# Optimization experiments

Measured on AMD Instinct MI355X. Metric: run time of the kernel, lower is better.

The kernel has to match this reference:

```python
import jax, jax.numpy as jnp
import numpy as np

B, D, H, E, TOPK = 65536, 1024, 512, 8, 2
LN_EPS = 1e-5
LB_WEIGHT = 0.01


def setup_inputs() -> dict:
    key = jax.random.key(0)
    ks = jax.random.split(key, 5)
    x = jax.random.normal(ks[0], (B, D), dtype=jnp.float32)
    W1 = jax.random.normal(ks[1], (D, H), dtype=jnp.float32) * 0.02
    b1 = jnp.zeros((H,), dtype=jnp.float32)
    ln_w = jnp.ones((H,), dtype=jnp.float32)
    ln_b = jnp.zeros((H,), dtype=jnp.float32)
    W2 = jax.random.normal(ks[2], (H, E), dtype=jnp.float32) * 0.02
    b2 = jnp.zeros((E,), dtype=jnp.float32)
    return {"x": x, "W1": W1, "b1": b1, "ln_w": ln_w, "ln_b": ln_b, "W2": W2, "b2": b2}


def _gate_logits(x, W1, b1, ln_w, ln_b, W2, b2):
    h = x @ W1 + b1                     # [B, H]
    mu = jnp.mean(h, axis=-1, keepdims=True)
    var = jnp.mean(jnp.square(h - mu), axis=-1, keepdims=True)
    h = (h - mu) * jax.lax.rsqrt(var + LN_EPS) * ln_w + ln_b
    h = jax.nn.gelu(h, approximate=False)  # torch nn.GELU default = exact erf
    return h @ W2 + b2                  # [B, E]


def reference(x, W1, b1, ln_w, ln_b, W2, b2):
    logits = _gate_logits(x, W1, b1, ln_w, ln_b, W2, b2)
    # sparse top-K routing (eval mode: no exploration noise)
    vals, idx = jax.lax.top_k(logits, TOPK)           # [B, K]
    rows = jnp.arange(logits.shape[0])[:, None]
    sparse = jnp.full_like(logits, -jnp.inf).at[rows, idx].set(vals)
    weights = jax.nn.softmax(sparse, axis=-1)         # zeros off top-k
    # Switch-style load-balance loss
    f = (weights > 0).astype(weights.dtype).mean(axis=0)  # fraction routed per expert
    P = weights.mean(axis=0)                              # mean gate prob per expert
    lb_loss = LB_WEIGHT * (E * jnp.sum(f * P))
    return weights, lb_loss
```

## Files before the change

kernel.cpp:

```cpp
#include <hip/hip_runtime.h>
#include <cstdint>
#include <cstddef>


typedef _Float16 f16;
typedef _Float16 f16x8 __attribute__((ext_vector_type(8)));
typedef float f32x4 __attribute__((ext_vector_type(4)));

#define B_ROWS 65536
#define D_DIM 1024
#define H_DIM 512
#define E_DIM 8
#define BM 64
#define BK 32
#define THREADS 256
#define NCHUNK 32
#define LDPX 40
#define SLABH 2560
#define BUFH 5120
#define IMG_CH (H_DIM * BK)
#define IMG_TOTAL (32 * IMG_CH)
#define GACC_OFF ((size_t)2 * IMG_TOTAL * sizeof(f16))

__global__ void prep_split(const float* __restrict__ W1,
                           f16* __restrict__ wh, f16* __restrict__ wl) {
  int id = blockIdx.x * 256 + threadIdx.x;
  int h = id & (H_DIM - 1);
  int kg = id >> 9;
  int c = kg >> 2;
  int kk0 = (kg & 3) * 8;
  int k0 = kg * 8;
  f16x8 hv, lv;
#pragma unroll
  for (int j = 0; j < 8; ++j) {
    float v = W1[(size_t)(k0 + j) * H_DIM + h] * 64.0f;
    f16 hi = (f16)v;
    hv[j] = hi;
    lv[j] = (f16)((v - (float)hi) * 256.0f);
  }
  size_t o = (size_t)c * IMG_CH + (size_t)h * BK + kk0;
  *(f16x8*)&wh[o] = hv;
  *(f16x8*)&wl[o] = lv;
}

__global__ void zero_acc(float* __restrict__ acc) {
  if (threadIdx.x < 16) acc[threadIdx.x] = 0.0f;
}

__global__ __launch_bounds__(THREADS, 2) void fused_main(
    const float* __restrict__ x,
    const f16* __restrict__ wh, const f16* __restrict__ wl,
    const float* __restrict__ b1, const float* __restrict__ lnw,
    const float* __restrict__ lnb, const float* __restrict__ W2,
    const float* __restrict__ b2, float* __restrict__ out,
    float* __restrict__ gacc) {
  __shared__ __align__(16) char pool[35584];
  f16* sx = (f16*)pool;

  const int tid = threadIdx.x;
  const int lane = tid & 63;
  const int wv = tid >> 6;
  const int l15 = lane & 15;
  const int l4 = lane >> 4;
  const int64_t row0 = (int64_t)blockIdx.x * BM;

  const int srow = tid >> 2;
  const int koff = (tid & 3) * 8;
  const int swo = srow * LDPX + koff;
  const float* xbase = x + (row0 + srow) * D_DIM + koff;

  const f16* whp = wh + (wv * 128 + l15) * BK + l4 * 8;

  f32x4 acc[4][8];
#pragma unroll
  for (int m = 0; m < 4; ++m)
#pragma unroll
    for (int n = 0; n < 8; ++n) acc[m][n] = (f32x4){0.f, 0.f, 0.f, 0.f};

  f16x8 setB[2][8];

#define ISSUE(si, C, half)                                                    \
  do {                                                                        \
    const f16* p = whp + (size_t)((C) & 31) * IMG_CH + (half) * 2048;         \
    setB[si][0] = *(const f16x8*)(p);                                         \
    setB[si][1] = *(const f16x8*)(p + 512);                                   \
    setB[si][2] = *(const f16x8*)(p + 1024);                                  \
    setB[si][3] = *(const f16x8*)(p + 1536);                                  \
    setB[si][4] = *(const f16x8*)(p + IMG_TOTAL);                             \
    setB[si][5] = *(const f16x8*)(p + IMG_TOTAL + 512);                       \
    setB[si][6] = *(const f16x8*)(p + IMG_TOTAL + 1024);                      \
    setB[si][7] = *(const f16x8*)(p + IMG_TOTAL + 1536);                      \
  } while (0)

#define CH_M(si, NH, bufv, MM)                                                \
  do {                                                                        \
    const int ao = (bufv)*BUFH + ((MM)*16 + l15) * LDPX + l4 * 8;             \
    f16x8 ah = *(const f16x8*)&sx[ao];                                        \
    f16x8 al = *(const f16x8*)&sx[ao + SLABH];                                \
    f16x8 ahs;                                                                \
    _Pragma("unroll") for (int q = 0; q < 8; ++q) ahs[q] =                    \
        ah[q] * (f16)0.00390625f;                                             \
    _Pragma("unroll") for (int n = 0; n < 4; ++n)                             \
      acc[MM][(NH)*4 + n] = __builtin_amdgcn_mfma_f32_16x16x32_f16(           \
          ah, setB[si][n], acc[MM][(NH)*4 + n], 0, 0, 0);                     \
    _Pragma("unroll") for (int n = 0; n < 4; ++n)                             \
      acc[MM][(NH)*4 + n] = __builtin_amdgcn_mfma_f32_16x16x32_f16(           \
          al, setB[si][n], acc[MM][(NH)*4 + n], 0, 0, 0);                     \
    _Pragma("unroll") for (int n = 0; n < 4; ++n)                             \
      acc[MM][(NH)*4 + n] = __builtin_amdgcn_mfma_f32_16x16x32_f16(           \
          ahs, setB[si][4 + n], acc[MM][(NH)*4 + n], 0, 0, 0);                \
  } while (0)

#define HALF(si, NH, bufv)                                                    \
  do {                                                                        \
    __builtin_amdgcn_s_setprio(1);                                            \
    CH_M(si, NH, bufv, 0);                                                    \
    CH_M(si, NH, bufv, 1);                                                    \
    CH_M(si, NH, bufv, 2);                                                    \
    CH_M(si, NH, bufv, 3);                                                    \
    __builtin_amdgcn_s_setprio(0);                                            \
  } while (0)

#define WRITE_SLAB(bufv)                                                      \
  do {                                                                        \
    float vv[8] = {xv0.x, xv0.y, xv0.z, xv0.w, xv1.x, xv1.y, xv1.z, xv1.w};   \
    f16x8 hv, lv;                                                             \
    _Pragma("unroll") for (int q = 0; q < 8; ++q) {                           \
      float t = vv[q] * 64.0f;                                                \
      f16 hh = (f16)t;                                                        \
      hv[q] = hh;                                                             \
      lv[q] = (f16)(t - (float)hh);                                           \
    }                                                                         \
    *(f16x8*)&sx[(bufv)*BUFH + swo] = hv;                                     \
    *(f16x8*)&sx[(bufv)*BUFH + SLABH + swo] = lv;                             \
  } while (0)

#define SLAB_BARRIER()                                                        \
  do {                                                                        \
    asm volatile("s_waitcnt lgkmcnt(0)" ::: "memory");                        \
    __builtin_amdgcn_s_barrier();                                             \
    __builtin_amdgcn_sched_barrier(0);                                        \
  } while (0)

  float4 xv0 = *(const float4*)(xbase);
  float4 xv1 = *(const float4*)(xbase + 4);
  WRITE_SLAB(0);
  ISSUE(0, 0, 0);
  ISSUE(1, 0, 1);
  xv0 = *(const float4*)(xbase + 32);
  xv1 = *(const float4*)(xbase + 36);
  SLAB_BARRIER();

  for (int c = 0; c < NCHUNK; ++c) {
    const int buf = c & 1;
    HALF(0, 0, buf);
    ISSUE(0, c + 1, 0);
    HALF(1, 1, buf);
    ISSUE(1, c + 1, 1);
    WRITE_SLAB(buf ^ 1);
    xv0 = *(const float4*)(xbase + ((c + 2) & 31) * 32);
    xv1 = *(const float4*)(xbase + ((c + 2) & 31) * 32 + 4);
    SLAB_BARRIER();
  }
#undef ISSUE
#undef CH_M
#undef HALF
#undef WRITE_SLAB
#undef SLAB_BARRIER
  __syncthreads();

  float* eW2T = (float*)pool;
  float* eStat = (float*)(pool + 24576);
  float* eLog = (float*)(pool + 26624);
  float* eMu = (float*)(pool + 34816);
  float* eRs = (float*)(pool + 35072);
  float* eFP = (float*)(pool + 35328);

  for (int i = tid; i < H_DIM; i += THREADS) {
    float4 wa = *(const float4*)&W2[i * 8];
    float4 wb = *(const float4*)&W2[i * 8 + 4];
    *(float4*)&eW2T[i * 12] = wa;
    *(float4*)&eW2T[i * 12 + 4] = wb;
  }
  if (tid < 16) eFP[tid] = 0.0f;

  float bb[8], lw[8], lb[8];
#pragma unroll
  for (int n = 0; n < 8; ++n) {
    int col = wv * 128 + n * 16 + l15;
    bb[n] = b1[col] * 4096.0f;
    lw[n] = lnw[col];
    lb[n] = lnb[col];
#pragma unroll
    for (int m = 0; m < 4; ++m)
#pragma unroll
      for (int r = 0; r < 4; ++r) acc[m][n][r] += bb[n];
  }

#pragma unroll
  for (int m = 0; m < 4; ++m) {
    float s1[4] = {0, 0, 0, 0};
    float s2[4] = {0, 0, 0, 0};
#pragma unroll
    for (int n = 0; n < 8; ++n)
#pragma unroll
      for (int r = 0; r < 4; ++r) {
        float vv = acc[m][n][r];
        s1[r] += vv;
        s2[r] = fmaf(vv, vv, s2[r]);
      }
#pragma unroll
    for (int d = 1; d < 16; d <<= 1)
#pragma unroll
      for (int r = 0; r < 4; ++r) {
        s1[r] += __shfl_xor(s1[r], d);
        s2[r] += __shfl_xor(s2[r], d);
      }
    if (l15 == 0) {
      int rb = m * 16 + l4 * 4;
#pragma unroll
      for (int r = 0; r < 4; ++r) {
        eStat[(wv * 64 + rb + r) * 2 + 0] = s1[r];
        eStat[(wv * 64 + rb + r) * 2 + 1] = s2[r];
      }
    }
  }
  __syncthreads();
  if (tid < BM) {
    float s1 = 0.0f, s2 = 0.0f;
#pragma unroll
    for (int w = 0; w < 4; ++w) {
      s1 += eStat[(w * 64 + tid) * 2 + 0];
      s2 += eStat[(w * 64 + tid) * 2 + 1];
    }
    float mu = s1 * (1.0f / 512.0f);
    float var = s2 * (1.0f / 512.0f) - mu * mu;
    eMu[tid] = mu;
    eRs[tid] = 1.0f / sqrtf(var + (1e-5f * 4096.0f * 4096.0f));
  }
  __syncthreads();

#pragma unroll
  for (int m = 0; m < 4; ++m) {
    int rb = m * 16 + l4 * 4;
#pragma unroll
    for (int r = 0; r < 4; ++r) {
      float mu_r = eMu[rb + r];
      float rs_r = eRs[rb + r];
      float lg[8];
#pragma unroll
      for (int e = 0; e < 8; ++e) lg[e] = 0.0f;
#pragma unroll
      for (int n = 0; n < 8; ++n) {
        int col = wv * 128 + n * 16 + l15;
        float hn = (acc[m][n][r] - mu_r) * rs_r;
        float y = fmaf(hn, lw[n], lb[n]);
        float g = 0.5f * y * (1.0f + erff(y * 0.70710678118654752440f));
        float4 w0 = *(const float4*)&eW2T[col * 12];
        float4 w1 = *(const float4*)&eW2T[col * 12 + 4];
        lg[0] = fmaf(g, w0.x, lg[0]);
        lg[1] = fmaf(g, w0.y, lg[1]);
        lg[2] = fmaf(g, w0.z, lg[2]);
        lg[3] = fmaf(g, w0.w, lg[3]);
        lg[4] = fmaf(g, w1.x, lg[4]);
        lg[5] = fmaf(g, w1.y, lg[5]);
        lg[6] = fmaf(g, w1.z, lg[6]);
        lg[7] = fmaf(g, w1.w, lg[7]);
      }
#pragma unroll
      for (int d = 1; d < 16; d <<= 1)
#pragma unroll
        for (int e = 0; e < 8; ++e) lg[e] += __shfl_xor(lg[e], d);
      if (l15 == 0) {
#pragma unroll
        for (int e = 0; e < 8; ++e) eLog[(wv * 64 + rb + r) * 8 + e] = lg[e];
      }
    }
  }
  __syncthreads();

  if (tid < BM) {
    float v[8];
#pragma unroll
    for (int e = 0; e < 8; ++e) {
      float s = b2[e];
#pragma unroll
      for (int w = 0; w < 4; ++w) s += eLog[(w * 64 + tid) * 8 + e];
      v[e] = s;
    }
    float m1 = v[0];
    int i1 = 0;
#pragma unroll
    for (int e = 1; e < 8; ++e)
      if (v[e] > m1) { m1 = v[e]; i1 = e; }
    float m2 = -3.0e38f;
    int i2 = -1;
#pragma unroll
    for (int e = 0; e < 8; ++e)
      if (e != i1 && v[e] > m2) { m2 = v[e]; i2 = e; }
    float dd = expf(m2 - m1);
    float inv = 1.0f / (1.0f + dd);
    float wA = inv, wB = dd * inv;
    float o[8];
#pragma unroll
    for (int e = 0; e < 8; ++e)
      o[e] = (e == i1) ? wA : ((e == i2) ? wB : 0.0f);
    float4* op = (float4*)&out[(row0 + tid) * 8];
    op[0] = (float4){o[0], o[1], o[2], o[3]};
    op[1] = (float4){o[4], o[5], o[6], o[7]};
    atomicAdd(&eFP[i1], 1.0f);
    atomicAdd(&eFP[i2], 1.0f);
    atomicAdd(&eFP[8 + i1], wA);
    atomicAdd(&eFP[8 + i2], wB);
  }
  __syncthreads();
  if (tid < 16) atomicAdd(&gacc[tid], eFP[tid]);
}

__global__ void lb_final(const float* __restrict__ gacc, float* __restrict__ out) {
  if (threadIdx.x == 0) {
    const float invB = 1.0f / 65536.0f;
    float s = 0.0f;
#pragma unroll
    for (int e = 0; e < 8; ++e) s += (gacc[e] * invB) * (gacc[8 + e] * invB);
    out[(size_t)B_ROWS * E_DIM] = 0.01f * 8.0f * s;
  }
}

extern "C" void kernel_launch(void* const* d_in, const int* in_sizes, int n_in,
                              void* d_out, int out_size, void* d_ws, size_t ws_size,
                              hipStream_t stream) {
  (void)in_sizes; (void)n_in; (void)out_size; (void)ws_size;
  const float* x = (const float*)d_in[0];
  const float* W1 = (const float*)d_in[1];
  const float* b1 = (const float*)d_in[2];
  const float* lnw = (const float*)d_in[3];
  const float* lnb = (const float*)d_in[4];
  const float* W2 = (const float*)d_in[5];
  const float* b2 = (const float*)d_in[6];
  float* out = (float*)d_out;
  f16* wh = (f16*)d_ws;
  f16* wl = wh + IMG_TOTAL;
  float* gacc = (float*)((char*)d_ws + GACC_OFF);

  zero_acc<<<1, 64, 0, stream>>>(gacc);
  prep_split<<<(D_DIM * H_DIM / 8) / 256, 256, 0, stream>>>(W1, wh, wl);
  fused_main<<<B_ROWS / BM, THREADS, 0, stream>>>(x, wh, wl, b1, lnw, lnb, W2, b2,
                                                  out, gacc);
  lb_final<<<1, 64, 0, stream>>>(gacc, out);
}
```

Before: 242.4 us.

## Load x directly into per-wave registers, dropping LDS staging and barriers

Each wave now loads its own A-operand fragments of x straight from global memory and splits them into high/low fp16 in registers, instead of cooperatively staging x through double-buffered LDS with a barrier per chunk. This removes the LDS writes and reads and the per-chunk block synchronisation. The cost is that all four waves redundantly load the same 64 rows of x (4x global/L2 traffic), and the loads are no longer prefetched a chunk ahead, so their latency may be exposed before the MFMAs.

```diff
diff --git a/kernel.cpp b/kernel.cpp
--- a/kernel.cpp
+++ b/kernel.cpp
@@ -15,9 +15,6 @@
 #define BK 32
 #define THREADS 256
 #define NCHUNK 32
-#define LDPX 40
-#define SLABH 2560
-#define BUFH 5120
 #define IMG_CH (H_DIM * BK)
 #define IMG_TOTAL (32 * IMG_CH)
 #define GACC_OFF ((size_t)2 * IMG_TOTAL * sizeof(f16))
@@ -55,7 +52,6 @@
     const float* __restrict__ b2, float* __restrict__ out,
     float* __restrict__ gacc) {
   __shared__ __align__(16) char pool[35584];
-  f16* sx = (f16*)pool;
 
   const int tid = threadIdx.x;
   const int lane = tid & 63;
@@ -64,10 +60,7 @@
   const int l4 = lane >> 4;
   const int64_t row0 = (int64_t)blockIdx.x * BM;
 
-  const int srow = tid >> 2;
-  const int koff = (tid & 3) * 8;
-  const int swo = srow * LDPX + koff;
-  const float* xbase = x + (row0 + srow) * D_DIM + koff;
+  const float* pax = x + (row0 + l15) * D_DIM + l4 * 8;
 
   const f16* whp = wh + (wv * 128 + l15) * BK + l4 * 8;
 
@@ -92,81 +85,59 @@
     setB[si][7] = *(const f16x8*)(p + IMG_TOTAL + 1536);                      \
   } while (0)
 
-#define CH_M(si, NH, bufv, MM)                                                \
+#define CH_M(si, NH, MM)                                                      \
   do {                                                                        \
-    const int ao = (bufv)*BUFH + ((MM)*16 + l15) * LDPX + l4 * 8;             \
-    f16x8 ah = *(const f16x8*)&sx[ao];                                        \
-    f16x8 al = *(const f16x8*)&sx[ao + SLABH];                                \
     f16x8 ahs;                                                                \
     _Pragma("unroll") for (int q = 0; q < 8; ++q) ahs[q] =                    \
-        ah[q] * (f16)0.00390625f;                                             \
+        ahf[MM][q] * (f16)0.00390625f;                                        \
     _Pragma("unroll") for (int n = 0; n < 4; ++n)                             \
       acc[MM][(NH)*4 + n] = __builtin_amdgcn_mfma_f32_16x16x32_f16(           \
-          ah, setB[si][n], acc[MM][(NH)*4 + n], 0, 0, 0);                     \
+          ahf[MM], setB[si][n], acc[MM][(NH)*4 + n], 0, 0, 0);                \
     _Pragma("unroll") for (int n = 0; n < 4; ++n)                             \
       acc[MM][(NH)*4 + n] = __builtin_amdgcn_mfma_f32_16x16x32_f16(           \
-          al, setB[si][n], acc[MM][(NH)*4 + n], 0, 0, 0);                     \
+          alf[MM], setB[si][n], acc[MM][(NH)*4 + n], 0, 0, 0);                \
     _Pragma("unroll") for (int n = 0; n < 4; ++n)                             \
       acc[MM][(NH)*4 + n] = __builtin_amdgcn_mfma_f32_16x16x32_f16(           \
           ahs, setB[si][4 + n], acc[MM][(NH)*4 + n], 0, 0, 0);                \
   } while (0)
 
-#define HALF(si, NH, bufv)                                                    \
+#define HALF(si, NH)                                                          \
   do {                                                                        \
     __builtin_amdgcn_s_setprio(1);                                            \
-    CH_M(si, NH, bufv, 0);                                                    \
-    CH_M(si, NH, bufv, 1);                                                    \
-    CH_M(si, NH, bufv, 2);                                                    \
-    CH_M(si, NH, bufv, 3);                                                    \
+    CH_M(si, NH, 0);                                                          \
+    CH_M(si, NH, 1);                                                          \
+    CH_M(si, NH, 2);                                                          \
+    CH_M(si, NH, 3);                                                          \
     __builtin_amdgcn_s_setprio(0);                                            \
   } while (0)
 
-#define WRITE_SLAB(bufv)                                                      \
-  do {                                                                        \
-    float vv[8] = {xv0.x, xv0.y, xv0.z, xv0.w, xv1.x, xv1.y, xv1.z, xv1.w};   \
-    f16x8 hv, lv;                                                             \
-    _Pragma("unroll") for (int q = 0; q < 8; ++q) {                           \
-      float t = vv[q] * 64.0f;                                                \
-      f16 hh = (f16)t;                                                        \
-      hv[q] = hh;                                                             \
-      lv[q] = (f16)(t - (float)hh);                                           \
-    }                                                                         \
-    *(f16x8*)&sx[(bufv)*BUFH + swo] = hv;                                     \
-    *(f16x8*)&sx[(bufv)*BUFH + SLABH + swo] = lv;                             \
-  } while (0)
-
-#define SLAB_BARRIER()                                                        \
-  do {                                                                        \
-    asm volatile("s_waitcnt lgkmcnt(0)" ::: "memory");                        \
-    __builtin_amdgcn_s_barrier();                                             \
-    __builtin_amdgcn_sched_barrier(0);                                        \
-  } while (0)
-
-  float4 xv0 = *(const float4*)(xbase);
-  float4 xv1 = *(const float4*)(xbase + 4);
-  WRITE_SLAB(0);
   ISSUE(0, 0, 0);
   ISSUE(1, 0, 1);
-  xv0 = *(const float4*)(xbase + 32);
-  xv1 = *(const float4*)(xbase + 36);
-  SLAB_BARRIER();
-
+
+  f16x8 ahf[4], alf[4];
   for (int c = 0; c < NCHUNK; ++c) {
-    const int buf = c & 1;
-    HALF(0, 0, buf);
+#pragma unroll
+    for (int m = 0; m < 4; ++m) {
+      const float* p = pax + m * (16 * D_DIM) + c * BK;
+      float4 v0 = *(const float4*)p;
+      float4 v1 = *(const float4*)(p + 4);
+      float vv[8] = {v0.x, v0.y, v0.z, v0.w, v1.x, v1.y, v1.z, v1.w};
+#pragma unroll
+      for (int q = 0; q < 8; ++q) {
+        float t = vv[q] * 64.0f;
+        f16 hh = (f16)t;
+        ahf[m][q] = hh;
+        alf[m][q] = (f16)(t - (float)hh);
+      }
+    }
+    HALF(0, 0);
     ISSUE(0, c + 1, 0);
-    HALF(1, 1, buf);
+    HALF(1, 1);
     ISSUE(1, c + 1, 1);
-    WRITE_SLAB(buf ^ 1);
-    xv0 = *(const float4*)(xbase + ((c + 2) & 31) * 32);
-    xv1 = *(const float4*)(xbase + ((c + 2) & 31) * 32 + 4);
-    SLAB_BARRIER();
   }
 #undef ISSUE
 #undef CH_M
 #undef HALF
-#undef WRITE_SLAB
-#undef SLAB_BARRIER
   __syncthreads();
 
   float* eW2T = (float*)pool;
```

Measured after the change: 328.2 us. 1.35x slower.
